# Performance work log

Hardware: AMD Instinct MI355X
Metric: run time of the kernel (lower is better)

The kernel has to match this reference:

```python
import jax, jax.numpy as jnp
import numpy as np

H, W, F, V, D = 1024, 1024, 100000, 50000, 32


def setup_inputs() -> dict:
    key = jax.random.key(0)
    k1, k2, k3, k4 = jax.random.split(key, 4)
    pix_to_face = jax.random.randint(k1, (H, W), 0, F, dtype=jnp.int64 if jax.config.read('jax_enable_x64') else jnp.int32)
    bg = jax.random.uniform(k2, (H, W)) < 0.1
    pix_to_face = jnp.where(bg, -1, pix_to_face)
    bary = jax.random.uniform(k2, (H, W, 3), dtype=jnp.float32)
    bary_coords = bary / jnp.sum(bary, axis=-1, keepdims=True)  # barycentric: sums to 1
    faces = jax.random.randint(k3, (F, 3), 0, V, dtype=pix_to_face.dtype)
    attributes = jax.random.normal(k4, (V, D), dtype=jnp.float32)
    return {"pix_to_face": pix_to_face, "bary_coords": bary_coords,
            "faces": faces, "attributes": attributes}


def reference(pix_to_face, bary_coords, faces, attributes):
    # faces[pix_to_face]: (H, W, 3) vertex indices (torch -1 wraps to last face)
    vertices_idx = jnp.take(faces, pix_to_face, axis=0, mode='wrap')
    # attributes[vertices_idx]: (H, W, 3, D)
    vertex_attribute = jnp.take(attributes, vertices_idx, axis=0, mode='wrap')
    # barycentric weighted sum over the 3 face vertices -> (H, W, D)
    attribute_map = jnp.einsum('hwk,hwkd->hwd', bary_coords, vertex_attribute)
    mask = pix_to_face != -1
    return attribute_map, mask
```

## Files before the change

### kernel.cpp

```cpp
#include <hip/hip_runtime.h>
#include <hip/hip_bf16.h>


typedef float fvec4 __attribute__((ext_vector_type(4)));
typedef unsigned short usvec8 __attribute__((ext_vector_type(8)));

__device__ __forceinline__ float bf16_to_f32(unsigned short h) {
    unsigned int u = ((unsigned int)h) << 16;
    return __builtin_bit_cast(float, u);
}

__global__ __launch_bounds__(256) void Renderer_prep_kernel(
    const float* __restrict__ attr, const int* __restrict__ faces,
    unsigned short* __restrict__ attr16, unsigned short* __restrict__ faces16,
    int nattr, int nfidx)
{
    int tid = blockIdx.x * blockDim.x + threadIdx.x;
    if (tid < nattr) {
        unsigned int u = __builtin_bit_cast(unsigned int, attr[tid]);
        unsigned int r = (u + 0x7FFFu + ((u >> 16) & 1u)) >> 16;
        attr16[tid] = (unsigned short)r;
    } else if (tid < nattr + nfidx) {
        int i = tid - nattr;
        faces16[i] = (unsigned short)faces[i];
    }
}

__global__ __launch_bounds__(256) void Renderer_interp16_kernel(
    const int* __restrict__ pix,
    const float* __restrict__ bary,
    const unsigned short* __restrict__ faces16,
    const usvec8* __restrict__ A,
    float* __restrict__ out,
    float* __restrict__ mask,
    int npix, int F)
{
    int tid = blockIdx.x * blockDim.x + threadIdx.x;
    int p = tid >> 2;
    int t = tid & 3;
    if (p >= npix) return;

    int fraw = __builtin_nontemporal_load(&pix[p]);
    int f = (fraw < 0) ? (fraw + F) : fraw;

    int b = 3 * f;
    int v0 = faces16[b + 0];
    int v1 = faces16[b + 1];
    int v2 = faces16[b + 2];

    float w0 = __builtin_nontemporal_load(&bary[3 * p + 0]);
    float w1 = __builtin_nontemporal_load(&bary[3 * p + 1]);
    float w2 = __builtin_nontemporal_load(&bary[3 * p + 2]);

    usvec8 r0 = A[v0 * 4 + t];
    usvec8 r1 = A[v1 * 4 + t];
    usvec8 r2 = A[v2 * 4 + t];

    fvec4 lo, hi;
    #pragma unroll
    for (int j = 0; j < 4; ++j) {
        float x = w0 * bf16_to_f32(r0[j]) + w1 * bf16_to_f32(r1[j])
                + w2 * bf16_to_f32(r2[j]);
        lo[j] = x;
    }
    #pragma unroll
    for (int j = 0; j < 4; ++j) {
        float x = w0 * bf16_to_f32(r0[j + 4]) + w1 * bf16_to_f32(r1[j + 4])
                + w2 * bf16_to_f32(r2[j + 4]);
        hi[j] = x;
    }

    fvec4* O = reinterpret_cast<fvec4*>(out);
    __builtin_nontemporal_store(lo, &O[(size_t)p * 8 + t * 2 + 0]);
    __builtin_nontemporal_store(hi, &O[(size_t)p * 8 + t * 2 + 1]);

    if (t == 0) {
        __builtin_nontemporal_store((fraw != -1) ? 1.0f : 0.0f, &mask[p]);
    }
}

__global__ __launch_bounds__(256) void Renderer_interp_kernel(
    const int* __restrict__ pix, const float* __restrict__ bary,
    const int* __restrict__ faces, const float* __restrict__ attr,
    float* __restrict__ out, float* __restrict__ mask, int npix, int F)
{
    int tid = blockIdx.x * blockDim.x + threadIdx.x;
    int p = tid >> 3;
    int t = tid & 7;
    if (p >= npix) return;
    int fraw = pix[p];
    int f = (fraw < 0) ? (fraw + F) : fraw;
    int base = 3 * f;
    int v0 = faces[base + 0], v1 = faces[base + 1], v2 = faces[base + 2];
    float w0 = bary[3 * p + 0], w1 = bary[3 * p + 1], w2 = bary[3 * p + 2];
    const fvec4* A = reinterpret_cast<const fvec4*>(attr);
    fvec4 r0 = A[v0 * 8 + t], r1 = A[v1 * 8 + t], r2 = A[v2 * 8 + t];
    fvec4 o = w0 * r0 + w1 * r1 + w2 * r2;
    reinterpret_cast<fvec4*>(out)[(size_t)p * 8 + t] = o;
    if (t == 0) mask[p] = (fraw != -1) ? 1.0f : 0.0f;
}

extern "C" void kernel_launch(void* const* d_in, const int* in_sizes, int n_in,
                              void* d_out, int out_size, void* d_ws, size_t ws_size,
                              hipStream_t stream) {
    const int*   pix   = (const int*)d_in[0];
    const float* bary  = (const float*)d_in[1];
    const int*   faces = (const int*)d_in[2];
    const float* attr  = (const float*)d_in[3];

    int npix  = in_sizes[0];
    int nfidx = in_sizes[2];
    int nattr = in_sizes[3];
    int F     = nfidx / 3;

    float* out  = (float*)d_out;
    float* mask = (float*)d_out + (size_t)npix * 32;

    size_t attr16_bytes = (size_t)nattr * sizeof(unsigned short);
    size_t need = attr16_bytes + (size_t)nfidx * sizeof(unsigned short);

    if (ws_size >= need) {
        unsigned short* attr16  = (unsigned short*)d_ws;
        unsigned short* faces16 = (unsigned short*)((char*)d_ws + attr16_bytes);

        int nprep = nattr + nfidx;
        Renderer_prep_kernel<<<(nprep + 255) / 256, 256, 0, stream>>>(
            attr, faces, attr16, faces16, nattr, nfidx);

        int total = npix * 4;
        Renderer_interp16_kernel<<<(total + 255) / 256, 256, 0, stream>>>(
            pix, bary, faces16, (const usvec8*)attr16, out, mask, npix, F);
    } else {
        int total = npix * 8;
        Renderer_interp_kernel<<<(total + 255) / 256, 256, 0, stream>>>(
            pix, bary, faces, attr, out, mask, npix, F);
    }
}
```

Baseline: 72.32 us.

## Split face lookup into separate pass writing packed 16-bit vertex indices

```diff
diff --git a/kernel.cpp b/kernel.cpp
--- a/kernel.cpp
+++ b/kernel.cpp
@@ -4,6 +4,7 @@
 
 typedef float fvec4 __attribute__((ext_vector_type(4)));
 typedef unsigned short usvec8 __attribute__((ext_vector_type(8)));
+typedef unsigned short usvec4 __attribute__((ext_vector_type(4)));
 
 __device__ __forceinline__ float bf16_to_f32(unsigned short h) {
     unsigned int u = ((unsigned int)h) << 16;
@@ -11,42 +12,57 @@
 }
 
 __global__ __launch_bounds__(256) void Renderer_prep_kernel(
-    const float* __restrict__ attr, const int* __restrict__ faces,
-    unsigned short* __restrict__ attr16, unsigned short* __restrict__ faces16,
-    int nattr, int nfidx)
+    const float* __restrict__ attr, unsigned short* __restrict__ attr16,
+    int nattr)
 {
     int tid = blockIdx.x * blockDim.x + threadIdx.x;
-    if (tid < nattr) {
-        unsigned int u = __builtin_bit_cast(unsigned int, attr[tid]);
-        unsigned int r = (u + 0x7FFFu + ((u >> 16) & 1u)) >> 16;
-        attr16[tid] = (unsigned short)r;
-    } else if (tid < nattr + nfidx) {
-        int i = tid - nattr;
-        faces16[i] = (unsigned short)faces[i];
-    }
+    if (tid >= nattr) return;
+    unsigned int u = __builtin_bit_cast(unsigned int, attr[tid]);
+    unsigned int r = (u + 0x7FFFu + ((u >> 16) & 1u)) >> 16;
+    attr16[tid] = (unsigned short)r;
 }
 
-__global__ __launch_bounds__(256) void Renderer_interp16_kernel(
+__global__ __launch_bounds__(256) void Renderer_passA_kernel(
     const int* __restrict__ pix,
+    const int* __restrict__ faces,
+    usvec4* __restrict__ vtx,
+    float* __restrict__ mask,
+    int npix, int F)
+{
+    int p = blockIdx.x * blockDim.x + threadIdx.x;
+    if (p >= npix) return;
+
+    int fraw = __builtin_nontemporal_load(&pix[p]);
+    int f = (fraw < 0) ? (fraw + F) : fraw;
+
+    int b = 3 * f;
+    int v0 = faces[b + 0];
+    int v1 = faces[b + 1];
+    int v2 = faces[b + 2];
+
+    usvec4 pk;
+    pk[0] = (unsigned short)v0;
+    pk[1] = (unsigned short)v1;
+    pk[2] = (unsigned short)v2;
+    pk[3] = 0;
+    __builtin_nontemporal_store(pk, &vtx[p]);
+    __builtin_nontemporal_store((fraw != -1) ? 1.0f : 0.0f, &mask[p]);
+}
+
+__global__ __launch_bounds__(256) void Renderer_passB_kernel(
+    const usvec4* __restrict__ vtx,
     const float* __restrict__ bary,
-    const unsigned short* __restrict__ faces16,
     const usvec8* __restrict__ A,
     float* __restrict__ out,
-    float* __restrict__ mask,
-    int npix, int F)
+    int npix)
 {
     int tid = blockIdx.x * blockDim.x + threadIdx.x;
     int p = tid >> 2;
     int t = tid & 3;
     if (p >= npix) return;
 
-    int fraw = __builtin_nontemporal_load(&pix[p]);
-    int f = (fraw < 0) ? (fraw + F) : fraw;
-
-    int b = 3 * f;
-    int v0 = faces16[b + 0];
-    int v1 = faces16[b + 1];
-    int v2 = faces16[b + 2];
+    usvec4 pk = __builtin_nontemporal_load(&vtx[p]);
+    int v0 = pk[0], v1 = pk[1], v2 = pk[2];
 
     float w0 = __builtin_nontemporal_load(&bary[3 * p + 0]);
     float w1 = __builtin_nontemporal_load(&bary[3 * p + 1]);
@@ -59,24 +75,15 @@
     fvec4 lo, hi;
     #pragma unroll
     for (int j = 0; j < 4; ++j) {
-        float x = w0 * bf16_to_f32(r0[j]) + w1 * bf16_to_f32(r1[j])
-                + w2 * bf16_to_f32(r2[j]);
-        lo[j] = x;
-    }
-    #pragma unroll
-    for (int j = 0; j < 4; ++j) {
-        float x = w0 * bf16_to_f32(r0[j + 4]) + w1 * bf16_to_f32(r1[j + 4])
-                + w2 * bf16_to_f32(r2[j + 4]);
-        hi[j] = x;
+        lo[j] = w0 * bf16_to_f32(r0[j]) + w1 * bf16_to_f32(r1[j])
+              + w2 * bf16_to_f32(r2[j]);
+        hi[j] = w0 * bf16_to_f32(r0[j + 4]) + w1 * bf16_to_f32(r1[j + 4])
+              + w2 * bf16_to_f32(r2[j + 4]);
     }
 
     fvec4* O = reinterpret_cast<fvec4*>(out);
     __builtin_nontemporal_store(lo, &O[(size_t)p * 8 + t * 2 + 0]);
     __builtin_nontemporal_store(hi, &O[(size_t)p * 8 + t * 2 + 1]);
-
-    if (t == 0) {
-        __builtin_nontemporal_store((fraw != -1) ? 1.0f : 0.0f, &mask[p]);
-    }
 }
 
 __global__ __launch_bounds__(256) void Renderer_interp_kernel(
@@ -117,19 +124,20 @@
     float* mask = (float*)d_out + (size_t)npix * 32;
 
     size_t attr16_bytes = (size_t)nattr * sizeof(unsigned short);
-    size_t need = attr16_bytes + (size_t)nfidx * sizeof(unsigned short);
+    size_t vtx_bytes    = (size_t)npix * sizeof(unsigned short) * 4;
+    size_t need = attr16_bytes + vtx_bytes;
 
     if (ws_size >= need) {
-        unsigned short* attr16  = (unsigned short*)d_ws;
-        unsigned short* faces16 = (unsigned short*)((char*)d_ws + attr16_bytes);
+        unsigned short* attr16 = (unsigned short*)d_ws;
+        usvec4* vtx = (usvec4*)((char*)d_ws + attr16_bytes);
 
-        int nprep = nattr + nfidx;
-        Renderer_prep_kernel<<<(nprep + 255) / 256, 256, 0, stream>>>(
-            attr, faces, attr16, faces16, nattr, nfidx);
-
+        Renderer_prep_kernel<<<(nattr + 255) / 256, 256, 0, stream>>>(
+            attr, attr16, nattr);
+        Renderer_passA_kernel<<<(npix + 255) / 256, 256, 0, stream>>>(
+            pix, faces, vtx, mask, npix, F);
         int total = npix * 4;
-        Renderer_interp16_kernel<<<(total + 255) / 256, 256, 0, stream>>>(
-            pix, bary, faces16, (const usvec8*)attr16, out, mask, npix, F);
+        Renderer_passB_kernel<<<(total + 255) / 256, 256, 0, stream>>>(
+            vtx, bary, (const usvec8*)attr16, out, npix);
     } else {
         int total = npix * 8;
         Renderer_interp_kernel<<<(total + 255) / 256, 256, 0, stream>>>(
```

New measurement: 71.05 us. About the same (-1.7%).
